# Kernel tuning notes

Measured on AMD Instinct MI355X. Metric: run time of the kernel, lower is better.

## Reference

```python
import jax, jax.numpy as jnp
import numpy as np

WS = 11          # window_size
SIGMA = 1.5
PAD = (WS - 1) // 2
C1 = (0.01 * 1.0) ** 2
C2 = (0.03 * 1.0) ** 2


def _gaussian_kernel2d():
    # kornia-style: 1D gaussian over window, normalized, outer product
    x = jnp.arange(WS, dtype=jnp.float32) - WS // 2
    g = jnp.exp(-(x ** 2) / (2.0 * SIGMA ** 2))
    g = g / jnp.sum(g)
    return jnp.outer(g, g)  # [WS, WS]


def _filter2d(x, k2d):
    # depthwise 2D filter with reflect ('same') padding, as kornia.filter2D
    b, c, h, w = x.shape
    xp = jnp.pad(x, ((0, 0), (0, 0), (PAD, PAD), (PAD, PAD)), mode='reflect')
    kern = jnp.broadcast_to(k2d.astype(x.dtype), (c, 1, WS, WS))
    return jax.lax.conv_general_dilated(
        xp, kern, window_strides=(1, 1), padding='VALID',
        feature_group_count=c,
        dimension_numbers=('NCHW', 'OIHW', 'NCHW'))


def setup_inputs() -> dict:
    key = jax.random.key(0)
    k1, k2 = jax.random.split(key)
    inp = jax.random.normal(k1, (16, 1, 1024, 1024), dtype=jnp.float32)
    tgt = jax.random.uniform(k2, (16, 1, 1024, 1024), dtype=jnp.float32)
    return {"input": inp, "target": tgt}


def reference(input, target):
    k2d = _gaussian_kernel2d()
    img1 = jax.nn.sigmoid(input)  # logsigmoid(x).exp() == sigmoid(x)
    img2 = target

    mu1 = _filter2d(img1, k2d)
    mu2 = _filter2d(img2, k2d)
    mu1_sq = mu1 * mu1
    mu2_sq = mu2 * mu2
    mu1_mu2 = mu1 * mu2

    sigma1_sq = _filter2d(img1 * img1, k2d) - mu1_sq
    sigma2_sq = _filter2d(img2 * img2, k2d) - mu2_sq
    sigma12 = _filter2d(img1 * img2, k2d) - mu1_mu2

    ssim_map = ((2.0 * mu1_mu2 + C1) * (2.0 * sigma12 + C2)) / (
        (mu1_sq + mu2_sq + C1) * (sigma1_sq + sigma2_sq + C2))
    loss = jnp.clip(1.0 - ssim_map, 0.0, 1.0) / 2.0
    return jnp.mean(loss)  # reduction='mean'
```

## Files before the change

### kernel.cpp

```cpp
#include <hip/hip_runtime.h>
#include <math.h>


typedef __attribute__((ext_vector_type(2))) float f2;

#define H_IMG 1024
#define W_IMG 1024
#define N_IMG 16
#define TILE_W 256
#define TILE_H 128
#define PADR 5
#define LDS_S2 268

constexpr float GW[11] = {
    0.00102838f, 0.00759877f, 0.03600077f, 0.10936069f, 0.21300553f,
    0.26601172f,
    0.21300553f, 0.10936069f, 0.03600077f, 0.00759877f, 0.00102838f};

__device__ __forceinline__ int reflect_i(int i, int n) {
    i = (i < 0) ? -i : i;
    i = (i >= n) ? (2 * n - 2 - i) : i;
    return i;
}

__device__ __forceinline__ float fast_sigmoid(float x) {
    return __builtin_amdgcn_rcpf(1.0f + __expf(-x));
}

__device__ __forceinline__ void ssim_emit(
    f2 mu, f2 sq, float e12, float& loss_sum)
{
    const float mu1 = mu.x, mu2 = mu.y;
    const float mu1s = mu1 * mu1;
    const float mu2s = mu2 * mu2;
    const float mu12 = mu1 * mu2;
    const float s1  = sq.x - mu1s;
    const float s2  = sq.y - mu2s;
    const float s12 = e12  - mu12;
    const float C1 = 1e-4f, C2 = 9e-4f;
    const float num = (2.0f * mu12 + C1) * (2.0f * s12 + C2);
    const float den = (mu1s + mu2s + C1) * (s1 + s2 + C2);
    float l = 1.0f - num * __builtin_amdgcn_rcpf(den);
    l = fminf(fmaxf(l, 0.0f), 1.0f) * 0.5f;
    loss_sum += l;
}

template<int NR>
__device__ __forceinline__ void load_group(
    const float* __restrict__ A, const float* __restrict__ B,
    int y_start, int gb, int c0, int c1, int tid,
    float (&pa)[11], float (&pb)[11], float (&pa2)[11], float (&pb2)[11])
{
#pragma unroll
    for (int r = 0; r < NR; ++r) {
        const int yy = reflect_i(y_start + gb + r, H_IMG);
        const size_t ro = (size_t)yy * W_IMG;
        pa[r] = A[ro + c0];
        pb[r] = B[ro + c0];
        if (tid < 2 * PADR) {
            pa2[r] = A[ro + c1];
            pb2[r] = B[ro + c1];
        }
    }
}

template<int NR>
__device__ __forceinline__ void write_group(
    f2 (*__restrict__ buf)[LDS_S2], int tid,
    const float (&pa)[11], const float (&pb)[11],
    const float (&pa2)[11], const float (&pb2)[11])
{
#pragma unroll
    for (int r = 0; r < NR; ++r) {
        buf[r][tid] = (f2){fast_sigmoid(pa[r]), pb[r]};
        if (tid < 2 * PADR)
            buf[r][TILE_W + tid] = (f2){fast_sigmoid(pa2[r]), pb2[r]};
    }
}

template<int NR, bool GUARD>
__device__ __forceinline__ void process_group(
    const f2 (*__restrict__ buf)[LDS_S2], int tid,
    f2 (&vAB)[11], f2 (&vSQ)[11], float (&vX)[11], float& loss_sum)
{
#pragma unroll
    for (int r = 0; r < NR; ++r) {
        f2 hAB = (f2)(0.0f), hSQ = (f2)(0.0f);
        float hab = 0.0f;
#pragma unroll
        for (int k = 0; k < 11; ++k) {
            const f2 v   = buf[r][tid + k];
            const f2 wa2 = ((f2)(GW[k])) * v;
            hAB += wa2;
            hSQ  = __builtin_elementwise_fma(wa2, v, hSQ);
            hab  = fmaf(wa2.x, v.y, hab);
        }
#pragma unroll
        for (int j = 0; j < 11; ++j) {
            if (!(GUARD && j > r)) {
                const int s = (r - j + 22) % 11;
                const f2 w2 = (f2)(GW[j]);
                vAB[s] = __builtin_elementwise_fma(w2, hAB, vAB[s]);
                vSQ[s] = __builtin_elementwise_fma(w2, hSQ, vSQ[s]);
                vX[s]  = fmaf(GW[j], hab, vX[s]);
            }
        }
        if (!GUARD || r == 10) {
            const int s = (r + 1) % 11;
            ssim_emit(vAB[s], vSQ[s], vX[s], loss_sum);
            vAB[s] = (f2)(0.0f); vSQ[s] = (f2)(0.0f); vX[s] = 0.0f;
        }
    }
}

__global__ __launch_bounds__(256, 2) void ssim_main(
    const float* __restrict__ inp, const float* __restrict__ tgt,
    float* __restrict__ out)
{
    __shared__ f2 bufs[2][11][LDS_S2];
    __shared__ float red[4];

    const int tid = threadIdx.x;
    const int blk = blockIdx.x;
    const int b   = blk >> 5;
    const int rem = blk & 31;
    const int cx  = rem & 3;
    const int ry  = rem >> 2;
    const int x0  = cx * TILE_W;
    const int y0  = ry * TILE_H;

    const float* __restrict__ A = inp + (size_t)b * (H_IMG * (size_t)W_IMG);
    const float* __restrict__ B = tgt + (size_t)b * (H_IMG * (size_t)W_IMG);

    const int c0 = reflect_i(x0 - PADR + tid, W_IMG);
    const int c1 = (tid < 2 * PADR) ? reflect_i(x0 + TILE_W - PADR + tid, W_IMG) : 0;

    f2 vAB[11], vSQ[11];
    float vX[11];
#pragma unroll
    for (int j = 0; j < 11; ++j) {
        vAB[j] = (f2)(0.0f); vSQ[j] = (f2)(0.0f); vX[j] = 0.0f;
    }
    float pa[11], pb[11], pa2[11], pb2[11];
    float loss_sum = 0.0f;

    const int y_start = y0 - PADR;

    load_group<11>(A, B, y_start, 0, c0, c1, tid, pa, pb, pa2, pb2);
    write_group<11>(bufs[0], tid, pa, pb, pa2, pb2);
    load_group<11>(A, B, y_start, 11, c0, c1, tid, pa, pb, pa2, pb2);
    __syncthreads();
    process_group<11, true>(bufs[0], tid, vAB, vSQ, vX, loss_sum);

#pragma unroll 1
    for (int g = 1; g <= 11; ++g) {
        f2 (*cur)[LDS_S2] = bufs[g & 1];
        write_group<11>(cur, tid, pa, pb, pa2, pb2);
        if (g <= 10)
            load_group<11>(A, B, y_start, (g + 1) * 11, c0, c1, tid, pa, pb, pa2, pb2);
        else
            load_group<6>(A, B, y_start, 132, c0, c1, tid, pa, pb, pa2, pb2);
        __syncthreads();
        process_group<11, false>(cur, tid, vAB, vSQ, vX, loss_sum);
    }

    write_group<6>(bufs[0], tid, pa, pb, pa2, pb2);
    __syncthreads();
    process_group<6, false>(bufs[0], tid, vAB, vSQ, vX, loss_sum);

#pragma unroll
    for (int off = 32; off > 0; off >>= 1)
        loss_sum += __shfl_down(loss_sum, off, 64);
    const int wave = tid >> 6;
    if ((tid & 63) == 0) red[wave] = loss_sum;
    __syncthreads();
    if (tid == 0) {
        const float s = red[0] + red[1] + red[2] + red[3];
        atomicAdd(out, s * (1.0f / ((float)N_IMG * H_IMG * W_IMG)));
    }
}

extern "C" void kernel_launch(void* const* d_in, const int* in_sizes, int n_in,
                              void* d_out, int out_size, void* d_ws, size_t ws_size,
                              hipStream_t stream) {
    const float* inp = (const float*)d_in[0];
    const float* tgt = (const float*)d_in[1];
    float* out = (float*)d_out;

    hipMemsetAsync(out, 0, sizeof(float), stream);

    const int grid = N_IMG * 4 * (H_IMG / TILE_H);
    ssim_main<<<grid, 256, 0, stream>>>(inp, tgt, out);
}
```

Measured before the change: 183.3 us.

## Give each wave its own column strip and LDS buffers, drop block barriers

Each of the four waves now owns a 64-column strip with private double-buffered LDS rows, so the per-group __syncthreads barriers are removed and waves run independently. The sigma1+sigma2 accumulators are merged into one channel because only their sum is used, which cuts the vertical-pass FMAs and registers. The cost is that each wave reloads a 10-column halo per strip instead of per 256-wide tile, so halo traffic and LDS footprint grow. It also relies on wave-synchronous ordering of LDS writes and reads with no barrier.

```diff
diff --git a/kernel.cpp b/kernel.cpp
--- a/kernel.cpp
+++ b/kernel.cpp
@@ -7,10 +7,10 @@
 #define H_IMG 1024
 #define W_IMG 1024
 #define N_IMG 16
-#define TILE_W 256
+#define WAVE_W 64
 #define TILE_H 128
 #define PADR 5
-#define LDS_S2 268
+#define LDS_S2 76
 
 constexpr float GW[11] = {
     0.00102838f, 0.00759877f, 0.03600077f, 0.10936069f, 0.21300553f,
@@ -28,18 +28,17 @@
 }
 
 __device__ __forceinline__ void ssim_emit(
-    f2 mu, f2 sq, float e12, float& loss_sum)
+    f2 mu, f2 sx, float& loss_sum)
 {
     const float mu1 = mu.x, mu2 = mu.y;
     const float mu1s = mu1 * mu1;
     const float mu2s = mu2 * mu2;
     const float mu12 = mu1 * mu2;
-    const float s1  = sq.x - mu1s;
-    const float s2  = sq.y - mu2s;
-    const float s12 = e12  - mu12;
+    const float ssum = sx.x - mu1s - mu2s;
+    const float s12  = sx.y - mu12;
     const float C1 = 1e-4f, C2 = 9e-4f;
     const float num = (2.0f * mu12 + C1) * (2.0f * s12 + C2);
-    const float den = (mu1s + mu2s + C1) * (s1 + s2 + C2);
+    const float den = (mu1s + mu2s + C1) * (ssum + C2);
     float l = 1.0f - num * __builtin_amdgcn_rcpf(den);
     l = fminf(fmaxf(l, 0.0f), 1.0f) * 0.5f;
     loss_sum += l;
@@ -48,16 +47,16 @@
 template<int NR>
 __device__ __forceinline__ void load_group(
     const float* __restrict__ A, const float* __restrict__ B,
-    int y_start, int gb, int c0, int c1, int tid,
+    int y_start, int gb, int c0, int c1, int lane,
     float (&pa)[11], float (&pb)[11], float (&pa2)[11], float (&pb2)[11])
 {
 #pragma unroll
     for (int r = 0; r < NR; ++r) {
         const int yy = reflect_i(y_start + gb + r, H_IMG);
-        const size_t ro = (size_t)yy * W_IMG;
+        const size_t ro = (size_t)yy << 10;
         pa[r] = A[ro + c0];
         pb[r] = B[ro + c0];
-        if (tid < 2 * PADR) {
+        if (lane < 2 * PADR) {
             pa2[r] = A[ro + c1];
             pb2[r] = B[ro + c1];
         }
@@ -66,22 +65,22 @@
 
 template<int NR>
 __device__ __forceinline__ void write_group(
-    f2 (*__restrict__ buf)[LDS_S2], int tid,
+    f2 (*__restrict__ buf)[LDS_S2], int lane,
     const float (&pa)[11], const float (&pb)[11],
     const float (&pa2)[11], const float (&pb2)[11])
 {
 #pragma unroll
     for (int r = 0; r < NR; ++r) {
-        buf[r][tid] = (f2){fast_sigmoid(pa[r]), pb[r]};
-        if (tid < 2 * PADR)
-            buf[r][TILE_W + tid] = (f2){fast_sigmoid(pa2[r]), pb2[r]};
+        buf[r][lane] = (f2){fast_sigmoid(pa[r]), pb[r]};
+        if (lane < 2 * PADR)
+            buf[r][WAVE_W + lane] = (f2){fast_sigmoid(pa2[r]), pb2[r]};
     }
 }
 
 template<int NR, bool GUARD>
 __device__ __forceinline__ void process_group(
-    const f2 (*__restrict__ buf)[LDS_S2], int tid,
-    f2 (&vAB)[11], f2 (&vSQ)[11], float (&vX)[11], float& loss_sum)
+    const f2 (*__restrict__ buf)[LDS_S2], int lane,
+    f2 (&vAB)[11], f2 (&vSX)[11], float& loss_sum)
 {
 #pragma unroll
     for (int r = 0; r < NR; ++r) {
@@ -89,26 +88,26 @@
         float hab = 0.0f;
 #pragma unroll
         for (int k = 0; k < 11; ++k) {
-            const f2 v   = buf[r][tid + k];
+            const f2 v   = buf[r][lane + k];
             const f2 wa2 = ((f2)(GW[k])) * v;
             hAB += wa2;
             hSQ  = __builtin_elementwise_fma(wa2, v, hSQ);
             hab  = fmaf(wa2.x, v.y, hab);
         }
+        const f2 hSX = (f2){hSQ.x + hSQ.y, hab};
 #pragma unroll
         for (int j = 0; j < 11; ++j) {
             if (!(GUARD && j > r)) {
                 const int s = (r - j + 22) % 11;
                 const f2 w2 = (f2)(GW[j]);
                 vAB[s] = __builtin_elementwise_fma(w2, hAB, vAB[s]);
-                vSQ[s] = __builtin_elementwise_fma(w2, hSQ, vSQ[s]);
-                vX[s]  = fmaf(GW[j], hab, vX[s]);
+                vSX[s] = __builtin_elementwise_fma(w2, hSX, vSX[s]);
             }
         }
         if (!GUARD || r == 10) {
             const int s = (r + 1) % 11;
-            ssim_emit(vAB[s], vSQ[s], vX[s], loss_sum);
-            vAB[s] = (f2)(0.0f); vSQ[s] = (f2)(0.0f); vX[s] = 0.0f;
+            ssim_emit(vAB[s], vSX[s], loss_sum);
+            vAB[s] = (f2)(0.0f); vSX[s] = (f2)(0.0f);
         }
     }
 }
@@ -117,62 +116,62 @@
     const float* __restrict__ inp, const float* __restrict__ tgt,
     float* __restrict__ out)
 {
-    __shared__ f2 bufs[2][11][LDS_S2];
+    __shared__ f2 lds[4][2][11][LDS_S2];
     __shared__ float red[4];
 
-    const int tid = threadIdx.x;
-    const int blk = blockIdx.x;
-    const int b   = blk >> 5;
-    const int rem = blk & 31;
-    const int cx  = rem & 3;
-    const int ry  = rem >> 2;
-    const int x0  = cx * TILE_W;
-    const int y0  = ry * TILE_H;
+    const int tid  = threadIdx.x;
+    const int lane = tid & 63;
+    const int w    = tid >> 6;
+    const int blk  = blockIdx.x;
+    const int b    = blk >> 5;
+    const int rem  = blk & 31;
+    const int ry   = rem >> 2;
+    const int cs   = (rem & 3) * 4 + w;
+    const int x0   = cs * WAVE_W;
+    const int y0   = ry * TILE_H;
 
     const float* __restrict__ A = inp + (size_t)b * (H_IMG * (size_t)W_IMG);
     const float* __restrict__ B = tgt + (size_t)b * (H_IMG * (size_t)W_IMG);
 
-    const int c0 = reflect_i(x0 - PADR + tid, W_IMG);
-    const int c1 = (tid < 2 * PADR) ? reflect_i(x0 + TILE_W - PADR + tid, W_IMG) : 0;
+    const int c0 = reflect_i(x0 - PADR + lane, W_IMG);
+    const int c1 = (lane < 2 * PADR)
+                       ? reflect_i(x0 + WAVE_W - PADR + lane, W_IMG) : 0;
 
-    f2 vAB[11], vSQ[11];
-    float vX[11];
+    f2 vAB[11], vSX[11];
 #pragma unroll
     for (int j = 0; j < 11; ++j) {
-        vAB[j] = (f2)(0.0f); vSQ[j] = (f2)(0.0f); vX[j] = 0.0f;
+        vAB[j] = (f2)(0.0f); vSX[j] = (f2)(0.0f);
     }
     float pa[11], pb[11], pa2[11], pb2[11];
     float loss_sum = 0.0f;
 
     const int y_start = y0 - PADR;
 
-    load_group<11>(A, B, y_start, 0, c0, c1, tid, pa, pb, pa2, pb2);
-    write_group<11>(bufs[0], tid, pa, pb, pa2, pb2);
-    load_group<11>(A, B, y_start, 11, c0, c1, tid, pa, pb, pa2, pb2);
-    __syncthreads();
-    process_group<11, true>(bufs[0], tid, vAB, vSQ, vX, loss_sum);
+    load_group<11>(A, B, y_start, 0, c0, c1, lane, pa, pb, pa2, pb2);
+    write_group<11>(lds[w][0], lane, pa, pb, pa2, pb2);
+    load_group<11>(A, B, y_start, 11, c0, c1, lane, pa, pb, pa2, pb2);
+    process_group<11, true>(lds[w][0], lane, vAB, vSX, loss_sum);
 
 #pragma unroll 1
     for (int g = 1; g <= 11; ++g) {
-        f2 (*cur)[LDS_S2] = bufs[g & 1];
-        write_group<11>(cur, tid, pa, pb, pa2, pb2);
+        f2 (*cur)[LDS_S2] = lds[w][g & 1];
+        write_group<11>(cur, lane, pa, pb, pa2, pb2);
         if (g <= 10)
-            load_group<11>(A, B, y_start, (g + 1) * 11, c0, c1, tid, pa, pb, pa2, pb2);
+            load_group<11>(A, B, y_start, (g + 1) * 11, c0, c1, lane,
+                           pa, pb, pa2, pb2);
         else
-            load_group<6>(A, B, y_start, 132, c0, c1, tid, pa, pb, pa2, pb2);
-        __syncthreads();
-        process_group<11, false>(cur, tid, vAB, vSQ, vX, loss_sum);
+            load_group<6>(A, B, y_start, 132, c0, c1, lane,
+                          pa, pb, pa2, pb2);
+        process_group<11, false>(cur, lane, vAB, vSX, loss_sum);
     }
 
-    write_group<6>(bufs[0], tid, pa, pb, pa2, pb2);
-    __syncthreads();
-    process_group<6, false>(bufs[0], tid, vAB, vSQ, vX, loss_sum);
+    write_group<6>(lds[w][0], lane, pa, pb, pa2, pb2);
+    process_group<6, false>(lds[w][0], lane, vAB, vSX, loss_sum);
 
 #pragma unroll
     for (int off = 32; off > 0; off >>= 1)
         loss_sum += __shfl_down(loss_sum, off, 64);
-    const int wave = tid >> 6;
-    if ((tid & 63) == 0) red[wave] = loss_sum;
+    if (lane == 0) red[w] = loss_sum;
     __syncthreads();
     if (tid == 0) {
         const float s = red[0] + red[1] + red[2] + red[3];
```

Result: no change. 183.2 us (-0.1%).
